# Performance work log

Measured on AMD Instinct MI355X. Metric: run time of the kernel, lower is better.

## Reference

```python
import jax, jax.numpy as jnp
import numpy as np

N_CAM, C, H, W = 4, 336, 96, 176
D, HB, WB = 6, 240, 120

def setup_inputs() -> dict:
    key = jax.random.key(0)
    k1, k2, k3, k4, k5 = jax.random.split(key, 5)
    return {
        "input": jax.random.normal(k1, (N_CAM, C, H, W), dtype=jnp.float32),
        "projection_u": jax.random.randint(k2, (N_CAM, D, HB, WB), 0, W, dtype=jnp.int32),
        "projection_v": jax.random.randint(k3, (N_CAM, D, HB, WB), 0, H, dtype=jnp.int32),
        "projection_valid": jax.random.randint(k4, (N_CAM, D, HB, WB), 0, 2, dtype=jnp.int32),
        "projection_density": jax.random.uniform(k5, (N_CAM, D, HB, WB), dtype=jnp.float32),
    }

def reference(input, projection_u, projection_v, projection_valid, projection_density):
    """Project2Dto3D: per-voxel gather from each camera feature map at (v,u),
    masked by validity and weighted by density normalization, summed over cameras.
    Output layout: [1, D*C, HB, WB] (336*6 = 2016 channels)."""
    def gather_cam(feat, u, v, valid, dens):
        # feat: (C,H,W); u,v,valid,dens: (D,HB,WB)
        g = feat[:, v, u]                                   # (C,D,HB,WB) gather
        w = valid.astype(feat.dtype) * dens                 # (D,HB,WB)
        return g * w[None]
    per_cam = jax.vmap(gather_cam)(input, projection_u, projection_v,
                                   projection_valid, projection_density)  # (N,C,D,HB,WB)
    out = per_cam.sum(axis=0)                               # (C,D,HB,WB)
    out = jnp.transpose(out, (1, 0, 2, 3))                  # (D,C,HB,WB)
    return out.reshape(1, D * C, HB, WB)
```

## Files before the change

kernel.cpp:

```cpp
#include <hip/hip_runtime.h>

#define NCAM 4
#define C 336
#define H 96
#define W 176
#define D 6
#define HB 240
#define WB 120
#define HW (H * W)
#define CPB 112
#define NPARTS 3
#define HALFROWS 56

static __device__ __forceinline__ unsigned short f2bf(float f) {
    unsigned u = __float_as_uint(f);
    unsigned r = (u + 0x7fffu + ((u >> 16) & 1u)) >> 16;
    return (unsigned short)r;
}

__global__ __launch_bounds__(256)
void vp_transpose_bf16(const float* __restrict__ in,
                       unsigned short* __restrict__ out) {
    __shared__ float tile[32][33];
    const int cam = blockIdx.z;
    const int hw0 = blockIdx.x * 32;
    const int c0  = blockIdx.y * 32;
    const int tx = threadIdx.x;
    const int ty = threadIdx.y;

    const float* src = in + (size_t)cam * C * HW;
#pragma unroll
    for (int k = 0; k < 32; k += 8) {
        int c = c0 + ty + k;
        if (c < C) tile[ty + k][tx] = src[(size_t)c * HW + (hw0 + tx)];
    }
    __syncthreads();

    unsigned* dst = (unsigned*)(out + (size_t)cam * HW * C);
    const int tid = ty * 32 + tx;
    const int cp     = tid & 15;
    const int hwbase = tid >> 4;
    const int c = c0 + cp * 2;
    if (c < C) {
#pragma unroll
        for (int k = 0; k < 2; ++k) {
            int hwl = hwbase + k * 16;
            unsigned ulo = f2bf(tile[cp * 2][hwl]);
            unsigned uhi = f2bf(tile[cp * 2 + 1][hwl]);
            dst[((size_t)(hw0 + hwl) * C + c) >> 1] = ulo | (uhi << 16);
        }
    }
}

__global__ __launch_bounds__(256, 4)
void vp_gather_bf16(const unsigned short* __restrict__ tfeat,
                    const int* __restrict__ pu, const int* __restrict__ pv,
                    const int* __restrict__ pvalid,
                    const float* __restrict__ pdens,
                    float* __restrict__ out) {
    __shared__ int   s_off[NCAM][WB];
    __shared__ float s_wgt[NCAM][WB];
    __shared__ float s_acc[HALFROWS][121];

    const int d     = blockIdx.x / HB;
    const int hb    = blockIdx.x % HB;
    const int cpart = blockIdx.y;
    const int tid   = threadIdx.x;

    for (int i = tid; i < NCAM * WB; i += 256) {
        int cam = i / WB, wb = i % WB;
        size_t pidx = ((size_t)(cam * D + d) * HB + hb) * WB + wb;
        float w = pvalid[pidx] ? pdens[pidx] : 0.0f;
        s_off[cam][wb] = cam * (HW * C) + (pv[pidx] * W + pu[pidx]) * C;
        s_wgt[cam][wb] = w;
    }
    __syncthreads();

    const int wave  = tid >> 6;
    const int lane  = tid & 63;
    const int cq    = lane >> 2;
    const int wbsub = lane & 3;
    const bool cact = (cq < 14);
    const int cbase = cpart * CPB + cq * 8;

    float acc[8][8];
#pragma unroll
    for (int i = 0; i < 8; ++i)
#pragma unroll
        for (int j = 0; j < 8; ++j) acc[i][j] = 0.0f;

#pragma unroll
    for (int wbi = 0; wbi < 8; ++wbi) {
        const int wbl = wbsub + 4 * wbi;
        const int wb  = wave * 30 + (wbl < 30 ? wbl : 29);
        const bool act = cact && (wbl < 30);
#pragma unroll
        for (int cam = 0; cam < NCAM; ++cam) {
            if (act) {
                const uint4 q = *(const uint4*)(tfeat + (size_t)s_off[cam][wb] + cbase);
                const float w = s_wgt[cam][wb];
                acc[wbi][0] += w * __uint_as_float(q.x << 16);
                acc[wbi][1] += w * __uint_as_float(q.x & 0xffff0000u);
                acc[wbi][2] += w * __uint_as_float(q.y << 16);
                acc[wbi][3] += w * __uint_as_float(q.y & 0xffff0000u);
                acc[wbi][4] += w * __uint_as_float(q.z << 16);
                acc[wbi][5] += w * __uint_as_float(q.z & 0xffff0000u);
                acc[wbi][6] += w * __uint_as_float(q.w << 16);
                acc[wbi][7] += w * __uint_as_float(q.w & 0xffff0000u);
            }
        }
    }

    for (int half = 0; half < 2; ++half) {
        if (cact && cq >= half * 7 && cq < half * 7 + 7) {
            const int rbase = (cq - half * 7) * 8;
#pragma unroll
            for (int wbi = 0; wbi < 8; ++wbi) {
                const int wbl = wbsub + 4 * wbi;
                if (wbl < 30) {
#pragma unroll
                    for (int j = 0; j < 8; ++j)
                        s_acc[rbase + j][wave * 30 + wbl] = acc[wbi][j];
                }
            }
        }
        __syncthreads();

        const int wb4 = tid & 31;
        const int rb  = tid >> 5;
        if (wb4 < 30) {
#pragma unroll
            for (int k = 0; k < 7; ++k) {
                const int r = rb + 8 * k;
                const int c = cpart * CPB + half * HALFROWS + r;
                float4 v;
                v.x = s_acc[r][wb4 * 4 + 0];
                v.y = s_acc[r][wb4 * 4 + 1];
                v.z = s_acc[r][wb4 * 4 + 2];
                v.w = s_acc[r][wb4 * 4 + 3];
                *(float4*)(out + (((size_t)d * C + c) * HB + hb) * WB + wb4 * 4) = v;
            }
        }
        __syncthreads();
    }
}

extern "C" void kernel_launch(void* const* d_in, const int* in_sizes, int n_in,
                              void* d_out, int out_size, void* d_ws,
                              size_t ws_size, hipStream_t stream) {
    const float* feat  = (const float*)d_in[0];
    const int* pu      = (const int*)d_in[1];
    const int* pv      = (const int*)d_in[2];
    const int* pvalid  = (const int*)d_in[3];
    const float* pdens = (const float*)d_in[4];
    float* out         = (float*)d_out;

    unsigned short* tfeat = (unsigned short*)d_ws;

    dim3 tgrid(HW / 32, (C + 31) / 32, NCAM);
    dim3 tblock(32, 8);
    vp_transpose_bf16<<<tgrid, tblock, 0, stream>>>(feat, tfeat);

    dim3 ggrid(D * HB, NPARTS);
    vp_gather_bf16<<<ggrid, 256, 0, stream>>>(tfeat, pu, pv, pvalid, pdens, out);
}
```

Measured before the change: 179.0 us.

## Vectorize transpose and split gather over width, dropping LDS output staging

The transpose kernel now reads float4 and writes 16-byte bf16 packs over 64-wide hw tiles. The gather kernel splits each row into two width halves (doubling the grid), issues all 16 feature loads up front for memory-level parallelism, and removes the branch predicate by clamping inactive lanes. Accumulators are written directly to global memory instead of being staged through shared memory for coalesced float4 stores, which removes two syncs and LDS traffic but makes the output stores strided and scalar.

```diff
diff --git a/kernel.cpp b/kernel.cpp
--- a/kernel.cpp
+++ b/kernel.cpp
@@ -9,8 +9,9 @@
 #define WB 120
 #define HW (H * W)
 #define CPB 112
-#define NPARTS 3
-#define HALFROWS 56
+#define WBPB 60
+#define NCP 3
+#define NWP 2
 
 static __device__ __forceinline__ unsigned short f2bf(float f) {
     unsigned u = __float_as_uint(f);
@@ -21,34 +22,41 @@
 __global__ __launch_bounds__(256)
 void vp_transpose_bf16(const float* __restrict__ in,
                        unsigned short* __restrict__ out) {
-    __shared__ float tile[32][33];
+    __shared__ float tile[64][33];
     const int cam = blockIdx.z;
-    const int hw0 = blockIdx.x * 32;
+    const int hw0 = blockIdx.x * 64;
     const int c0  = blockIdx.y * 32;
-    const int tx = threadIdx.x;
-    const int ty = threadIdx.y;
+    const int tid = threadIdx.x;
 
-    const float* src = in + (size_t)cam * C * HW;
+    const int hwq = tid & 15;
+    const int cl  = tid >> 4;
+    const float* src = in + (size_t)cam * C * HW + hw0 + hwq * 4;
 #pragma unroll
-    for (int k = 0; k < 32; k += 8) {
-        int c = c0 + ty + k;
-        if (c < C) tile[ty + k][tx] = src[(size_t)c * HW + (hw0 + tx)];
+    for (int cc = 0; cc < 2; ++cc) {
+        const int c = c0 + cl + cc * 16;
+        if (c < C) {
+            const float4 v = *(const float4*)(src + (size_t)c * HW);
+            tile[hwq * 4 + 0][cl + cc * 16] = v.x;
+            tile[hwq * 4 + 1][cl + cc * 16] = v.y;
+            tile[hwq * 4 + 2][cl + cc * 16] = v.z;
+            tile[hwq * 4 + 3][cl + cc * 16] = v.w;
+        }
     }
     __syncthreads();
 
-    unsigned* dst = (unsigned*)(out + (size_t)cam * HW * C);
-    const int tid = ty * 32 + tx;
-    const int cp     = tid & 15;
-    const int hwbase = tid >> 4;
-    const int c = c0 + cp * 2;
-    if (c < C) {
+    const int hw  = tid >> 2;
+    const int oct = tid & 3;
+    const int cs  = c0 + oct * 8;
+    if (cs < C) {
+        uint4 r;
+        unsigned* pr = (unsigned*)&r;
 #pragma unroll
-        for (int k = 0; k < 2; ++k) {
-            int hwl = hwbase + k * 16;
-            unsigned ulo = f2bf(tile[cp * 2][hwl]);
-            unsigned uhi = f2bf(tile[cp * 2 + 1][hwl]);
-            dst[((size_t)(hw0 + hwl) * C + c) >> 1] = ulo | (uhi << 16);
+        for (int k = 0; k < 4; ++k) {
+            unsigned lo = f2bf(tile[hw][oct * 8 + 2 * k]);
+            unsigned hi = f2bf(tile[hw][oct * 8 + 2 * k + 1]);
+            pr[k] = lo | (hi << 16);
         }
+        *(uint4*)(out + (size_t)cam * HW * C + (size_t)(hw0 + hw) * C + cs) = r;
     }
 }
 
@@ -58,21 +66,25 @@
                     const int* __restrict__ pvalid,
                     const float* __restrict__ pdens,
                     float* __restrict__ out) {
-    __shared__ int   s_off[NCAM][WB];
-    __shared__ float s_wgt[NCAM][WB];
-    __shared__ float s_acc[HALFROWS][121];
+    __shared__ int   s_off[NCAM][WBPB];
+    __shared__ float s_wgt[NCAM][WBPB];
 
-    const int d     = blockIdx.x / HB;
-    const int hb    = blockIdx.x % HB;
-    const int cpart = blockIdx.y;
-    const int tid   = threadIdx.x;
+    const int d      = blockIdx.x / HB;
+    const int hb     = blockIdx.x % HB;
+    const int cpart  = blockIdx.y % NCP;
+    const int wbpart = blockIdx.y / NCP;
+    const int wb0    = wbpart * WBPB;
+    const int tid    = threadIdx.x;
 
-    for (int i = tid; i < NCAM * WB; i += 256) {
-        int cam = i / WB, wb = i % WB;
-        size_t pidx = ((size_t)(cam * D + d) * HB + hb) * WB + wb;
-        float w = pvalid[pidx] ? pdens[pidx] : 0.0f;
-        s_off[cam][wb] = cam * (HW * C) + (pv[pidx] * W + pu[pidx]) * C;
-        s_wgt[cam][wb] = w;
+    {
+        const int i = tid;
+        if (i < NCAM * WBPB) {
+            const int cam = i / WBPB, wbl = i % WBPB;
+            const size_t pidx =
+                ((size_t)(cam * D + d) * HB + hb) * WB + wb0 + wbl;
+            s_wgt[cam][wbl] = pvalid[pidx] ? pdens[pidx] : 0.0f;
+            s_off[cam][wbl] = cam * (HW * C) + (pv[pidx] * W + pu[pidx]) * C;
+        }
     }
     __syncthreads();
 
@@ -81,67 +93,55 @@
     const int cq    = lane >> 2;
     const int wbsub = lane & 3;
     const bool cact = (cq < 14);
-    const int cbase = cpart * CPB + cq * 8;
+    const int cqc   = cact ? cq : 13;
+    const int cbase = cpart * CPB + cqc * 8;
 
-    float acc[8][8];
+    uint4 q[4][4];
+    int wbc[4];
 #pragma unroll
-    for (int i = 0; i < 8; ++i)
+    for (int wbi = 0; wbi < 4; ++wbi) {
+        const int wbl = wbsub + 4 * wbi;
+        wbc[wbi] = wave * 15 + (wbl < 15 ? wbl : 14);
+#pragma unroll
+        for (int cam = 0; cam < NCAM; ++cam) {
+            q[wbi][cam] =
+                *(const uint4*)(tfeat + (size_t)s_off[cam][wbc[wbi]] + cbase);
+        }
+    }
+
+    float acc[4][8];
+#pragma unroll
+    for (int i = 0; i < 4; ++i)
 #pragma unroll
         for (int j = 0; j < 8; ++j) acc[i][j] = 0.0f;
 
 #pragma unroll
-    for (int wbi = 0; wbi < 8; ++wbi) {
-        const int wbl = wbsub + 4 * wbi;
-        const int wb  = wave * 30 + (wbl < 30 ? wbl : 29);
-        const bool act = cact && (wbl < 30);
+    for (int wbi = 0; wbi < 4; ++wbi) {
 #pragma unroll
         for (int cam = 0; cam < NCAM; ++cam) {
-            if (act) {
-                const uint4 q = *(const uint4*)(tfeat + (size_t)s_off[cam][wb] + cbase);
-                const float w = s_wgt[cam][wb];
-                acc[wbi][0] += w * __uint_as_float(q.x << 16);
-                acc[wbi][1] += w * __uint_as_float(q.x & 0xffff0000u);
-                acc[wbi][2] += w * __uint_as_float(q.y << 16);
-                acc[wbi][3] += w * __uint_as_float(q.y & 0xffff0000u);
-                acc[wbi][4] += w * __uint_as_float(q.z << 16);
-                acc[wbi][5] += w * __uint_as_float(q.z & 0xffff0000u);
-                acc[wbi][6] += w * __uint_as_float(q.w << 16);
-                acc[wbi][7] += w * __uint_as_float(q.w & 0xffff0000u);
-            }
+            const float w = s_wgt[cam][wbc[wbi]];
+            const uint4 v = q[wbi][cam];
+            acc[wbi][0] += w * __uint_as_float(v.x << 16);
+            acc[wbi][1] += w * __uint_as_float(v.x & 0xffff0000u);
+            acc[wbi][2] += w * __uint_as_float(v.y << 16);
+            acc[wbi][3] += w * __uint_as_float(v.y & 0xffff0000u);
+            acc[wbi][4] += w * __uint_as_float(v.z << 16);
+            acc[wbi][5] += w * __uint_as_float(v.z & 0xffff0000u);
+            acc[wbi][6] += w * __uint_as_float(v.w << 16);
+            acc[wbi][7] += w * __uint_as_float(v.w & 0xffff0000u);
         }
     }
 
-    for (int half = 0; half < 2; ++half) {
-        if (cact && cq >= half * 7 && cq < half * 7 + 7) {
-            const int rbase = (cq - half * 7) * 8;
 #pragma unroll
-            for (int wbi = 0; wbi < 8; ++wbi) {
-                const int wbl = wbsub + 4 * wbi;
-                if (wbl < 30) {
+    for (int wbi = 0; wbi < 4; ++wbi) {
+        const int wbl = wbsub + 4 * wbi;
+        if (cact && wbl < 15) {
+            const int wb = wb0 + wave * 15 + wbl;
+            float* po = out + (((size_t)d * C + cbase) * HB + hb) * WB + wb;
 #pragma unroll
-                    for (int j = 0; j < 8; ++j)
-                        s_acc[rbase + j][wave * 30 + wbl] = acc[wbi][j];
-                }
-            }
+            for (int j = 0; j < 8; ++j)
+                po[(size_t)j * HB * WB] = acc[wbi][j];
         }
-        __syncthreads();
-
-        const int wb4 = tid & 31;
-        const int rb  = tid >> 5;
-        if (wb4 < 30) {
-#pragma unroll
-            for (int k = 0; k < 7; ++k) {
-                const int r = rb + 8 * k;
-                const int c = cpart * CPB + half * HALFROWS + r;
-                float4 v;
-                v.x = s_acc[r][wb4 * 4 + 0];
-                v.y = s_acc[r][wb4 * 4 + 1];
-                v.z = s_acc[r][wb4 * 4 + 2];
-                v.w = s_acc[r][wb4 * 4 + 3];
-                *(float4*)(out + (((size_t)d * C + c) * HB + hb) * WB + wb4 * 4) = v;
-            }
-        }
-        __syncthreads();
     }
 }
 
@@ -157,10 +157,10 @@
 
     unsigned short* tfeat = (unsigned short*)d_ws;
 
-    dim3 tgrid(HW / 32, (C + 31) / 32, NCAM);
-    dim3 tblock(32, 8);
-    vp_transpose_bf16<<<tgrid, tblock, 0, stream>>>(feat, tfeat);
+    dim3 tgrid(HW / 64, (C + 31) / 32, NCAM);
+    vp_transpose_bf16<<<tgrid, 256, 0, stream>>>(feat, tfeat);
 
-    dim3 ggrid(D * HB, NPARTS);
-    vp_gather_bf16<<<ggrid, 256, 0, stream>>>(tfeat, pu, pv, pvalid, pdens, out);
+    dim3 ggrid(D * HB, NCP * NWP);
+    vp_gather_bf16<<<ggrid, 256, 0, stream>>>(tfeat, pu, pv, pvalid, pdens,
+                                              out);
 }
```

Measured after the change: 199.9 us. +11.7%, slower.
